# Performance work log

Hardware: AMD Instinct MI355X
Metric: run time of the kernel (lower is better)

## Reference

```python
import jax, jax.numpy as jnp
import numpy as np

DIM = 256
WINDOW = 512  # look_backward=1, look_forward=0, causal


def setup_inputs() -> dict:
    key = jax.random.key(0)
    ks = jax.random.split(key, 7)
    B, N, D = 8, 8192, DIM
    s = D ** -0.5
    return {
        "x": jax.random.normal(ks[0], (B, D, N), dtype=jnp.float32),
        "Wq": jax.random.normal(ks[1], (D, D), dtype=jnp.float32) * s,
        "bq": jax.random.normal(ks[2], (D,), dtype=jnp.float32) * 0.01,
        "Wk": jax.random.normal(ks[3], (D, D), dtype=jnp.float32) * s,
        "bk": jax.random.normal(ks[4], (D,), dtype=jnp.float32) * 0.01,
        "Wv": jax.random.normal(ks[5], (D, D), dtype=jnp.float32) * s,
        "bv": jax.random.normal(ks[6], (D,), dtype=jnp.float32) * 0.01,
    }


def _local_attention(q, k, v, window):
    # q,k,v: (B, N, D); causal sliding-window attention, look_backward=1 window.
    b, n, d = q.shape
    nw = n // window  # N assumed multiple of window (autopad no-op here)
    scale = d ** -0.5
    qb = q.reshape(b, nw, window, d)
    kb = k.reshape(b, nw, window, d)
    vb = v.reshape(b, nw, window, d)

    def look_back(t):
        prev = jnp.pad(t, ((0, 0), (1, 0), (0, 0), (0, 0)))[:, :-1]
        return jnp.concatenate([prev, t], axis=2)  # (b, nw, 2*window, d)

    kb2 = look_back(kb)
    vb2 = look_back(vb)

    pos = jnp.arange(n).reshape(nw, window)
    prev_pos = jnp.pad(pos, ((1, 0), (0, 0)), constant_values=-1)[:-1]
    kpos = jnp.concatenate([prev_pos, pos], axis=1)  # (nw, 2*window)
    # causal mask + mask out the (nonexistent) window before window 0
    mask = (pos[:, :, None] >= kpos[:, None, :]) & (kpos[:, None, :] >= 0)

    scores = jnp.einsum('bnqd,bnkd->bnqk', qb, kb2) * scale
    scores = jnp.where(mask[None], scores, jnp.asarray(-1e9, scores.dtype))
    attn = jax.nn.softmax(scores, axis=-1)  # dropout(0.1) omitted: eval mode
    out = jnp.einsum('bnqk,bnkd->bnqd', attn, vb2)
    return out.reshape(b, n, d)


def reference(x, Wq, bq, Wk, bk, Wv, bv):
    # x: (B, D, N) -> permute -> (B, N, D)
    xp = jnp.transpose(x, (0, 2, 1))
    q = xp @ Wq.T + bq
    k = xp @ Wk.T + bk
    v = xp @ Wv.T + bv
    y = xp + _local_attention(q, k, v, WINDOW)  # residual
    return jnp.transpose(y, (0, 2, 1))
```

## Files before the change

### kernel.cpp

```cpp
#include <hip/hip_runtime.h>
#include <hip/hip_bf16.h>

#define DIM  256
#define NSEQ 8192
#define BATCH 8
#define WIN  512

typedef __attribute__((ext_vector_type(8))) short short8;
typedef __attribute__((ext_vector_type(4))) float floatx4;

union PFU { int i[4]; short8 v; };

__device__ __forceinline__ int packbf(float a, float b) {
    __hip_bfloat162 h;
    h.x = __float2bfloat16(a);
    h.y = __float2bfloat16(b);
    int r;
    __builtin_memcpy(&r, &h, 4);
    return r;
}

__device__ __forceinline__ void gld_lds16(void* lds_dst, const void* g_src) {
    __builtin_amdgcn_global_load_lds(
        (const __attribute__((address_space(1))) void*)g_src,
        (__attribute__((address_space(3))) void*)lds_dst,
        16, 0, 0);
}

__global__ __launch_bounds__(256) void k_transpose(const float* __restrict__ x,
                                                   __hip_bfloat16* __restrict__ xT) {
    __shared__ float tile[64][65];
    const int b  = blockIdx.z;
    const int n0 = blockIdx.x * 64;
    const int d0 = blockIdx.y * 64;
    const int t  = threadIdx.x;
    const int ln = t & 63, grp = t >> 6;

    const float* xb = x + (size_t)b * DIM * NSEQ;
#pragma unroll
    for (int i = 0; i < 16; ++i) {
        int d = grp * 16 + i;
        tile[d][ln] = xb[(size_t)(d0 + d) * NSEQ + n0 + ln];
    }
    __syncthreads();
    __hip_bfloat16* xTb = xT + (size_t)b * NSEQ * DIM;
    const int a2 = t & 15, nr = t >> 4;
#pragma unroll
    for (int i = 0; i < 4; ++i) {
        const int n = i * 16 + nr;
        union { __hip_bfloat16 h[4]; ushort4 u; } pk;
#pragma unroll
        for (int k = 0; k < 4; ++k)
            pk.h[k] = __float2bfloat16(tile[a2 * 4 + k][n]);
        *(ushort4*)(xTb + (size_t)(n0 + n) * DIM + d0 + a2 * 4) = pk.u;
    }
}

__global__ __launch_bounds__(256) void k_wcast(const float* __restrict__ w0,
                                               const float* __restrict__ w1,
                                               const float* __restrict__ w2,
                                               __hip_bfloat16* __restrict__ wb) {
    int i = (blockIdx.x * 256 + threadIdx.x) * 4;
    const float* s = (i < 65536) ? (w0 + i) : ((i < 131072) ? (w1 + i - 65536) : (w2 + i - 131072));
    float4 v = *(const float4*)s;
    union { __hip_bfloat16 h[4]; ushort4 u; } cv;
    cv.h[0] = __float2bfloat16(v.x);
    cv.h[1] = __float2bfloat16(v.y);
    cv.h[2] = __float2bfloat16(v.z);
    cv.h[3] = __float2bfloat16(v.w);
    *(ushort4*)(wb + i) = cv.u;
}

__global__ __launch_bounds__(256, 3) void k_proj(const __hip_bfloat16* __restrict__ xT,
                                                 const __hip_bfloat16* __restrict__ wb,
                                                 const float* __restrict__ bq,
                                                 const float* __restrict__ bk,
                                                 const float* __restrict__ bv,
                                                 __hip_bfloat16* __restrict__ qo,
                                                 __hip_bfloat16* __restrict__ ko,
                                                 __hip_bfloat16* __restrict__ vto) {
    __shared__ __align__(16) char As[32768];
    const int b   = blockIdx.y;
    const int m0  = blockIdx.x * 64;
    const int tid = threadIdx.x;
    const int wv  = tid >> 6;
    const int l   = tid & 63;
    const int lm  = l & 15;
    const int qd  = l >> 4;
    const int wn  = wv * 64;

    const char* Ap = (const char*)(xT + ((size_t)b * NSEQ + m0) * DIM);
#pragma unroll
    for (int ii = 0; ii < 8; ++ii) {
        const int ks = wv * 2 + (ii >> 2);
        const int r0 = (ii & 3) * 16;
        gld_lds16(As + ks * 4096 + r0 * 64,
                  Ap + (size_t)(r0 + (l >> 2)) * 512 + ks * 64 + (l & 3) * 16);
    }
    __syncthreads();

#pragma unroll
    for (int mode = 0; mode < 3; ++mode) {
        const __hip_bfloat16* wp = wb + mode * 65536;
        floatx4 acc[4][4];
#pragma unroll
        for (int i = 0; i < 4; ++i)
#pragma unroll
            for (int j = 0; j < 4; ++j) acc[i][j] = (floatx4){0.f, 0.f, 0.f, 0.f};

#pragma unroll
        for (int ks = 0; ks < 8; ++ks) {
            short8 wf[4], af[4];
#pragma unroll
            for (int j = 0; j < 4; ++j)
                wf[j] = *(const short8*)(wp + (size_t)(wn + j * 16 + lm) * DIM + ks * 32 + qd * 8);
#pragma unroll
            for (int j = 0; j < 4; ++j)
                af[j] = *(const short8*)(As + ks * 4096 + (j * 16 + lm) * 64 + qd * 16);
            if (mode < 2) {
#pragma unroll
                for (int mt = 0; mt < 4; ++mt)
#pragma unroll
                    for (int nt = 0; nt < 4; ++nt)
                        acc[mt][nt] = __builtin_amdgcn_mfma_f32_16x16x32_bf16(af[mt], wf[nt], acc[mt][nt], 0, 0, 0);
            } else {
#pragma unroll
                for (int jw = 0; jw < 4; ++jw)
#pragma unroll
                    for (int ja = 0; ja < 4; ++ja)
                        acc[jw][ja] = __builtin_amdgcn_mfma_f32_16x16x32_bf16(wf[jw], af[ja], acc[jw][ja], 0, 0, 0);
            }
        }

        if (mode < 2) {
            const float* bias = mode ? bk : bq;
            __hip_bfloat16* op = (mode ? ko : qo) + (size_t)b * NSEQ * DIM;
            float bc[4];
#pragma unroll
            for (int nt = 0; nt < 4; ++nt) bc[nt] = bias[wn + nt * 16 + lm];
#pragma unroll
            for (int mt = 0; mt < 4; ++mt)
#pragma unroll
                for (int nt = 0; nt < 4; ++nt)
#pragma unroll
                    for (int r = 0; r < 4; ++r)
                        op[(size_t)(m0 + mt * 16 + qd * 4 + r) * DIM + wn + nt * 16 + lm] =
                            __float2bfloat16(acc[mt][nt][r] + bc[nt]);
        } else {
            __hip_bfloat16* op = vto + (size_t)b * DIM * NSEQ;
#pragma unroll
            for (int jw = 0; jw < 4; ++jw)
#pragma unroll
                for (int r = 0; r < 4; ++r) {
                    const int d = wn + jw * 16 + qd * 4 + r;
                    const float bb = bv[d];
#pragma unroll
                    for (int ja = 0; ja < 4; ++ja)
                        op[(size_t)d * NSEQ + m0 + ja * 16 + lm] =
                            __float2bfloat16(acc[jw][ja][r] + bb);
                }
        }
    }
}

__global__ __launch_bounds__(512, 2) void k_attn(const __hip_bfloat16* __restrict__ qm,
                                                 const __hip_bfloat16* __restrict__ km,
                                                 const __hip_bfloat16* __restrict__ vtm,
                                                 const float* __restrict__ x,
                                                 float* __restrict__ out) {
    __shared__ __align__(16) char kbuf[2][16384];
    __shared__ __align__(16) char vbuf[2][16384];

    const int w  = blockIdx.x, b = blockIdx.y, qt = blockIdx.z;
    const int tid = threadIdx.x;
    const int wv = tid >> 6;
    const int l  = tid & 63;
    const int m  = l & 15;
    const int qd = l >> 4;

    const int qbw   = qt * 256 + wv * 32;
    const int koff0 = w * WIN - WIN;

    short8 qf[2][8];
#pragma unroll
    for (int u = 0; u < 2; ++u) {
        const __hip_bfloat16* qrow =
            qm + ((size_t)b * NSEQ + (size_t)(w * WIN + qbw + u * 16 + m)) * DIM;
#pragma unroll
        for (int s = 0; s < 8; ++s)
            qf[u][s] = *(const short8*)(qrow + s * 32 + qd * 8);
    }

    const char* kbase = (const char*)(km + (size_t)b * NSEQ * DIM);
    const char* vbase = (const char*)(vtm + (size_t)b * DIM * NSEQ);

    const int c0  = (w == 0) ? 16 : 0;
    const int c1w = (512 + qbw + 63) >> 5;
    const int c1b = (799 + qt * 256) >> 5;

    const bool   isK     = wv < 4;
    const size_t gstride = isK ? (size_t)64 : (size_t)16 * NSEQ * 2;
    const size_t adv     = isK ? (size_t)32 * 512 : (size_t)64;
    const int    lbase   = (isK ? wv * 4 : (wv - 4) * 4) * 1024 + l * 16;
    const char* gp0;
    if (isK)
        gp0 = kbase + (size_t)(koff0 + c0 * 32 + (wv >> 1) * 16 + m) * 512 +
              (size_t)((wv & 1) * 16 + qd) * 16;
    else
        gp0 = vbase + (size_t)((wv - 4) * 64 + m) * (NSEQ * 2) +
              (size_t)(koff0 + c0 * 32) * 2 + (size_t)qd * 16;

    floatx4 o[2][16];
#pragma unroll
    for (int u = 0; u < 2; ++u)
#pragma unroll
        for (int t = 0; t < 16; ++t) o[u][t] = (floatx4){0.f, 0.f, 0.f, 0.f};
    float mi[2] = {-INFINITY, -INFINITY};
    float li[2] = {0.f, 0.f};
    const float sscale = 0.0625f * 1.4426950408889634f;

    const int a0 = (((qd & 1) * 2) * 16 + m) * 4;
    const int a1 = a0 + 64;
    const bool hi = (qd >> 1) != 0;

    int4 rg[4];
#pragma unroll
    for (int i = 0; i < 4; ++i)
        rg[i] = *(const int4*)(gp0 + (size_t)i * gstride);
    gp0 += adv;
    {
        char* d0 = (isK ? kbuf[0] : vbuf[0]) + lbase;
#pragma unroll
        for (int i = 0; i < 4; ++i)
            *(int4*)(d0 + i * 1024) = rg[i];
    }
    __syncthreads();

    int pb = 0;
    for (int c = c0; c < c1b; ++c) {
        const bool more = (c + 1 < c1b);
        if (more) {
#pragma unroll
            for (int i = 0; i < 4; ++i)
                rg[i] = *(const int4*)(gp0 + (size_t)i * gstride);
            gp0 += adv;
        }
        if (c < c1w) {
            const char* kbp = kbuf[pb];
            floatx4 st[2][2];
#pragma unroll
            for (int u = 0; u < 2; ++u)
#pragma unroll
                for (int t = 0; t < 2; ++t) st[u][t] = (floatx4){0.f, 0.f, 0.f, 0.f};
            __builtin_amdgcn_s_setprio(1);
#pragma unroll
            for (int t = 0; t < 2; ++t)
#pragma unroll
                for (int s = 0; s < 8; ++s) {
                    short8 kf = *(const short8*)(kbp + ((t * 8 + s) * 64 + l) * 16);
                    st[0][t] = __builtin_amdgcn_mfma_f32_16x16x32_bf16(kf, qf[0][s], st[0][t], 0, 0, 0);
                    st[1][t] = __builtin_amdgcn_mfma_f32_16x16x32_bf16(kf, qf[1][s], st[1][t], 0, 0, 0);
                }
            __builtin_amdgcn_s_setprio(0);
            const int kl0 = c * 32;
            short8 pf[2];
#pragma unroll
            for (int u = 0; u < 2; ++u) {
                const int lim = 512 + qbw + u * 16 + m;
                const bool needmask = (kl0 + 31) > lim;
                float p[8];
#pragma unroll
                for (int t = 0; t < 2; ++t)
#pragma unroll
                    for (int r = 0; r < 4; ++r) {
                        float v = st[u][t][r] * sscale;
                        if (needmask) {
                            int key = kl0 + t * 16 + qd * 4 + r;
                            v = (key <= lim) ? v : -INFINITY;
                        }
                        p[t * 4 + r] = v;
                    }
                float mx = p[0];
#pragma unroll
                for (int i = 1; i < 8; ++i) mx = fmaxf(mx, p[i]);
                mx = fmaxf(mx, __shfl_xor(mx, 16, 64));
                mx = fmaxf(mx, __shfl_xor(mx, 32, 64));
                float mnew;
                if (__all(mx <= mi[u] + 8.0f)) mnew = mi[u];
                else                           mnew = fmaxf(mi[u], mx);
                const float alpha = exp2f(mi[u] - mnew);
                float ps = 0.f;
#pragma unroll
                for (int i = 0; i < 8; ++i) { p[i] = exp2f(p[i] - mnew); ps += p[i]; }
                ps += __shfl_xor(ps, 16, 64);
                ps += __shfl_xor(ps, 32, 64);
                li[u] = li[u] * alpha + ps;
                mi[u] = mnew;
                if (!__all(alpha == 1.0f)) {
#pragma unroll
                    for (int t = 0; t < 16; ++t) {
                        o[u][t][0] *= alpha; o[u][t][1] *= alpha;
                        o[u][t][2] *= alpha; o[u][t][3] *= alpha;
                    }
                }
                int pd0 = packbf(p[0], p[1]);
                int pd1 = packbf(p[2], p[3]);
                int pd2 = packbf(p[4], p[5]);
                int pd3 = packbf(p[6], p[7]);
                int x0 = __builtin_amdgcn_ds_bpermute(a0, pd0);
                int y0 = __builtin_amdgcn_ds_bpermute(a0, pd2);
                int x1 = __builtin_amdgcn_ds_bpermute(a0, pd1);
                int y1 = __builtin_amdgcn_ds_bpermute(a0, pd3);
                int x2 = __builtin_amdgcn_ds_bpermute(a1, pd0);
                int y2 = __builtin_amdgcn_ds_bpermute(a1, pd2);
                int x3 = __builtin_amdgcn_ds_bpermute(a1, pd1);
                int y3 = __builtin_amdgcn_ds_bpermute(a1, pd3);
                PFU pu;
                pu.i[0] = hi ? y0 : x0;
                pu.i[1] = hi ? y1 : x1;
                pu.i[2] = hi ? y2 : x2;
                pu.i[3] = hi ? y3 : x3;
                pf[u] = pu.v;
            }
            const char* vbp = vbuf[pb];
            __builtin_amdgcn_s_setprio(1);
#pragma unroll
            for (int t = 0; t < 16; ++t) {
                short8 vf = *(const short8*)(vbp + (t * 64 + l) * 16);
                o[0][t] = __builtin_amdgcn_mfma_f32_16x16x32_bf16(vf, pf[0], o[0][t], 0, 0, 0);
                o[1][t] = __builtin_amdgcn_mfma_f32_16x16x32_bf16(vf, pf[1], o[1][t], 0, 0, 0);
            }
            __builtin_amdgcn_s_setprio(0);
        }
        if (more) {
            char* dst = (isK ? kbuf[pb ^ 1] : vbuf[pb ^ 1]) + lbase;
#pragma unroll
            for (int i = 0; i < 4; ++i)
                *(int4*)(dst + i * 1024) = rg[i];
        }
        __syncthreads();
        pb ^= 1;
    }

#pragma unroll
    for (int u = 0; u < 2; ++u) {
        const float inv = 1.f / li[u];
        const int ng = w * WIN + qbw + u * 16 + m;
        const float* xr  = x   + (size_t)b * DIM * NSEQ + ng;
        float*       orw = out + (size_t)b * DIM * NSEQ + ng;
#pragma unroll
        for (int t = 0; t < 16; ++t)
#pragma unroll
            for (int r = 0; r < 4; ++r) {
                int d = t * 16 + qd * 4 + r;
                orw[(size_t)d * NSEQ] = xr[(size_t)d * NSEQ] + o[u][t][r] * inv;
            }
    }
}

extern "C" void kernel_launch(void* const* d_in, const int* in_sizes, int n_in,
                              void* d_out, int out_size, void* d_ws, size_t ws_size,
                              hipStream_t stream) {
    const float* x  = (const float*)d_in[0];
    const float* Wq = (const float*)d_in[1];
    const float* bq = (const float*)d_in[2];
    const float* Wk = (const float*)d_in[3];
    const float* bk = (const float*)d_in[4];
    const float* Wv = (const float*)d_in[5];
    const float* bv = (const float*)d_in[6];

    char* ws = (char*)d_ws;
    const size_t SZ = (size_t)BATCH * NSEQ * DIM * sizeof(__hip_bfloat16);
    __hip_bfloat16* xT  = (__hip_bfloat16*)(ws);
    __hip_bfloat16* qb_ = (__hip_bfloat16*)(ws + SZ);
    __hip_bfloat16* kb_ = (__hip_bfloat16*)(ws + 2 * SZ);
    __hip_bfloat16* vt_ = (__hip_bfloat16*)(ws + 3 * SZ);
    __hip_bfloat16* wb_ = (__hip_bfloat16*)(ws + 4 * SZ);

    k_transpose<<<dim3(NSEQ / 64, DIM / 64, BATCH), 256, 0, stream>>>(x, xT);
    k_wcast<<<dim3(192), 256, 0, stream>>>(Wq, Wk, Wv, wb_);
    k_proj<<<dim3(NSEQ / 64, BATCH), 256, 0, stream>>>(xT, wb_, bq, bk, bv, qb_, kb_, vt_);
    k_attn<<<dim3(16, BATCH, 2), 512, 0, stream>>>(qb_, kb_, vt_, x, (float*)d_out);
}
```

Baseline: 357.5 us.

## Fuse input transpose and bf16 cast into the QKV projection kernel

Removes the separate transpose kernel and its bf16 xT workspace. The projection kernel now loads fp32 x tiles directly, transposes them through an LDS staging tile, and packs them to bf16 in a new LDS layout for the MFMA A operand. This cuts a full write and re-read of the transposed activation plus one kernel launch. In exchange it uses more LDS per block and adds extra barriers in the projection prologue.

```diff
diff --git a/kernel.cpp b/kernel.cpp
--- a/kernel.cpp
+++ b/kernel.cpp
@@ -18,42 +18,6 @@
     int r;
     __builtin_memcpy(&r, &h, 4);
     return r;
-}
-
-__device__ __forceinline__ void gld_lds16(void* lds_dst, const void* g_src) {
-    __builtin_amdgcn_global_load_lds(
-        (const __attribute__((address_space(1))) void*)g_src,
-        (__attribute__((address_space(3))) void*)lds_dst,
-        16, 0, 0);
-}
-
-__global__ __launch_bounds__(256) void k_transpose(const float* __restrict__ x,
-                                                   __hip_bfloat16* __restrict__ xT) {
-    __shared__ float tile[64][65];
-    const int b  = blockIdx.z;
-    const int n0 = blockIdx.x * 64;
-    const int d0 = blockIdx.y * 64;
-    const int t  = threadIdx.x;
-    const int ln = t & 63, grp = t >> 6;
-
-    const float* xb = x + (size_t)b * DIM * NSEQ;
-#pragma unroll
-    for (int i = 0; i < 16; ++i) {
-        int d = grp * 16 + i;
-        tile[d][ln] = xb[(size_t)(d0 + d) * NSEQ + n0 + ln];
-    }
-    __syncthreads();
-    __hip_bfloat16* xTb = xT + (size_t)b * NSEQ * DIM;
-    const int a2 = t & 15, nr = t >> 4;
-#pragma unroll
-    for (int i = 0; i < 4; ++i) {
-        const int n = i * 16 + nr;
-        union { __hip_bfloat16 h[4]; ushort4 u; } pk;
-#pragma unroll
-        for (int k = 0; k < 4; ++k)
-            pk.h[k] = __float2bfloat16(tile[a2 * 4 + k][n]);
-        *(ushort4*)(xTb + (size_t)(n0 + n) * DIM + d0 + a2 * 4) = pk.u;
-    }
 }
 
 __global__ __launch_bounds__(256) void k_wcast(const float* __restrict__ w0,
@@ -71,7 +35,7 @@
     *(ushort4*)(wb + i) = cv.u;
 }
 
-__global__ __launch_bounds__(256, 3) void k_proj(const __hip_bfloat16* __restrict__ xT,
+__global__ __launch_bounds__(256, 3) void k_prep(const float* __restrict__ x,
                                                  const __hip_bfloat16* __restrict__ wb,
                                                  const float* __restrict__ bq,
                                                  const float* __restrict__ bk,
@@ -79,9 +43,10 @@
                                                  __hip_bfloat16* __restrict__ qo,
                                                  __hip_bfloat16* __restrict__ ko,
                                                  __hip_bfloat16* __restrict__ vto) {
+    __shared__ float ftile[64][68];
     __shared__ __align__(16) char As[32768];
     const int b   = blockIdx.y;
-    const int m0  = blockIdx.x * 64;
+    const int n0  = blockIdx.x * 64;
     const int tid = threadIdx.x;
     const int wv  = tid >> 6;
     const int l   = tid & 63;
@@ -89,15 +54,32 @@
     const int qd  = l >> 4;
     const int wn  = wv * 64;
 
-    const char* Ap = (const char*)(xT + ((size_t)b * NSEQ + m0) * DIM);
-#pragma unroll
-    for (int ii = 0; ii < 8; ++ii) {
-        const int ks = wv * 2 + (ii >> 2);
-        const int r0 = (ii & 3) * 16;
-        gld_lds16(As + ks * 4096 + r0 * 64,
-                  Ap + (size_t)(r0 + (l >> 2)) * 512 + ks * 64 + (l & 3) * 16);
-    }
-    __syncthreads();
+    const float* xb = x + (size_t)b * DIM * NSEQ;
+
+    const int dr = l >> 4, nseg = l & 15;
+#pragma unroll
+    for (int dsl = 0; dsl < 4; ++dsl) {
+        const int d0 = dsl * 64;
+#pragma unroll
+        for (int i = 0; i < 4; ++i) {
+            const int r = wv * 16 + i * 4 + dr;
+            float4 v = *(const float4*)(xb + (size_t)(d0 + r) * NSEQ + n0 + nseg * 4);
+            *(float4*)&ftile[r][nseg * 4] = v;
+        }
+        __syncthreads();
+#pragma unroll
+        for (int p = 0; p < 2; ++p) {
+            const int ks = dsl * 2 + p;
+            int4 pk;
+            int* pki = (int*)&pk;
+#pragma unroll
+            for (int jj = 0; jj < 4; ++jj)
+                pki[jj] = packbf(ftile[p * 32 + wv * 8 + jj * 2][l],
+                                 ftile[p * 32 + wv * 8 + jj * 2 + 1][l]);
+            *(int4*)(As + ks * 4096 + wv * 1024 + l * 16) = pk;
+        }
+        __syncthreads();
+    }
 
 #pragma unroll
     for (int mode = 0; mode < 3; ++mode) {
@@ -116,7 +98,7 @@
                 wf[j] = *(const short8*)(wp + (size_t)(wn + j * 16 + lm) * DIM + ks * 32 + qd * 8);
 #pragma unroll
             for (int j = 0; j < 4; ++j)
-                af[j] = *(const short8*)(As + ks * 4096 + (j * 16 + lm) * 64 + qd * 16);
+                af[j] = *(const short8*)(As + ks * 4096 + qd * 1024 + (j * 16 + lm) * 16);
             if (mode < 2) {
 #pragma unroll
                 for (int mt = 0; mt < 4; ++mt)
@@ -144,7 +126,7 @@
                 for (int nt = 0; nt < 4; ++nt)
 #pragma unroll
                     for (int r = 0; r < 4; ++r)
-                        op[(size_t)(m0 + mt * 16 + qd * 4 + r) * DIM + wn + nt * 16 + lm] =
+                        op[(size_t)(n0 + mt * 16 + qd * 4 + r) * DIM + wn + nt * 16 + lm] =
                             __float2bfloat16(acc[mt][nt][r] + bc[nt]);
         } else {
             __hip_bfloat16* op = vto + (size_t)b * DIM * NSEQ;
@@ -156,7 +138,7 @@
                     const float bb = bv[d];
 #pragma unroll
                     for (int ja = 0; ja < 4; ++ja)
-                        op[(size_t)d * NSEQ + m0 + ja * 16 + lm] =
+                        op[(size_t)d * NSEQ + n0 + ja * 16 + lm] =
                             __float2bfloat16(acc[jw][ja][r] + bb);
                 }
         }
@@ -371,14 +353,12 @@
 
     char* ws = (char*)d_ws;
     const size_t SZ = (size_t)BATCH * NSEQ * DIM * sizeof(__hip_bfloat16);
-    __hip_bfloat16* xT  = (__hip_bfloat16*)(ws);
-    __hip_bfloat16* qb_ = (__hip_bfloat16*)(ws + SZ);
-    __hip_bfloat16* kb_ = (__hip_bfloat16*)(ws + 2 * SZ);
-    __hip_bfloat16* vt_ = (__hip_bfloat16*)(ws + 3 * SZ);
-    __hip_bfloat16* wb_ = (__hip_bfloat16*)(ws + 4 * SZ);
-
-    k_transpose<<<dim3(NSEQ / 64, DIM / 64, BATCH), 256, 0, stream>>>(x, xT);
+    __hip_bfloat16* qb_ = (__hip_bfloat16*)(ws);
+    __hip_bfloat16* kb_ = (__hip_bfloat16*)(ws + SZ);
+    __hip_bfloat16* vt_ = (__hip_bfloat16*)(ws + 2 * SZ);
+    __hip_bfloat16* wb_ = (__hip_bfloat16*)(ws + 3 * SZ);
+
     k_wcast<<<dim3(192), 256, 0, stream>>>(Wq, Wk, Wv, wb_);
-    k_proj<<<dim3(NSEQ / 64, BATCH), 256, 0, stream>>>(xT, wb_, bq, bk, bv, qb_, kb_, vt_);
+    k_prep<<<dim3(NSEQ / 64, BATCH), 256, 0, stream>>>(x, wb_, bq, bk, bv, qb_, kb_, vt_);
     k_attn<<<dim3(16, BATCH, 2), 512, 0, stream>>>(qb_, kb_, vt_, x, (float*)d_out);
 }
```

New measurement: 347.6 us. 1.03x faster.
